# Kernel optimization log

Measured on AMD Instinct MI355X. Metric: run time of the kernel, lower is better.

Reference implementation:

```python
import jax, jax.numpy as jnp
import numpy as np

N = 100000      # nodes per node type
E = 500000      # edges per relation
DIN = 128
DOUT = 128
H = 8
DK = DOUT // H  # 16
SQRT_DK = float(np.sqrt(DK))


def setup_inputs() -> dict:
    key = jax.random.key(0)
    ks = jax.random.split(key, 24)
    s = 1.0 / np.sqrt(DIN)
    inp = {
        "h_a": jax.random.normal(ks[0], (N, DIN), jnp.float32),
        "h_b": jax.random.normal(ks[1], (N, DIN), jnp.float32),
        "src0": jax.random.randint(ks[2], (E,), 0, N, jnp.int32),
        "dst0": jax.random.randint(ks[3], (E,), 0, N, jnp.int32),
        "src1": jax.random.randint(ks[4], (E,), 0, N, jnp.int32),
        "dst1": jax.random.randint(ks[5], (E,), 0, N, jnp.int32),
        "src2": jax.random.randint(ks[6], (E,), 0, N, jnp.int32),
        "dst2": jax.random.randint(ks[7], (E,), 0, N, jnp.int32),
        "Wk": jax.random.normal(ks[8], (2, DIN, DOUT), jnp.float32) * s,
        "bk": jnp.zeros((2, DOUT), jnp.float32),
        "Wv": jax.random.normal(ks[9], (2, DIN, DOUT), jnp.float32) * s,
        "bv": jnp.zeros((2, DOUT), jnp.float32),
        "Wq": jax.random.normal(ks[10], (2, DIN, DOUT), jnp.float32) * s,
        "bq": jnp.zeros((2, DOUT), jnp.float32),
        "Wa": jax.random.normal(ks[11], (2, DOUT, DOUT), jnp.float32) * s,
        "ba": jnp.zeros((2, DOUT), jnp.float32),
        # xavier_uniform-like scale for [H, DK, DK] relation transforms
        "rel_att": jax.random.normal(ks[12], (3, H, DK, DK), jnp.float32) * (1.0 / np.sqrt(DK)),
        "rel_msg": jax.random.normal(ks[13], (3, H, DK, DK), jnp.float32) * (1.0 / np.sqrt(DK)),
        "rel_pri": 1.0 + 0.1 * jax.random.normal(ks[14], (3, H), jnp.float32),
        "skip": jnp.zeros((2,), jnp.float32),
    }
    return inp


def _relation(x_src, x_dst, src, dst, Wk_, bk_, Wv_, bv_, Wq_, bq_, att, msg, pri):
    """One canonical edge type: returns scatter-sum aggregation t [N, H, DK]."""
    k = (x_src @ Wk_ + bk_).reshape(-1, H, DK)
    k = jnp.einsum('nhd,hde->nhe', k, att)                     # relation-specific key transform
    v = jnp.einsum('nhd,hde->nhe', (x_src @ Wv_ + bv_).reshape(-1, H, DK), msg)
    q = (x_dst @ Wq_ + bq_).reshape(-1, H, DK)
    # per-edge dot-product score [E, H] (v_dot_u with q on dst, k on src)
    score = jnp.einsum('ehd,ehd->eh', q[dst], k[src]) * pri / SQRT_DK
    # edge softmax grouped by dst node
    smax = jax.ops.segment_max(score, dst, num_segments=N)
    smax = jnp.where(jnp.isfinite(smax), smax, 0.0)            # empty dst groups
    ex = jnp.exp(score - smax[dst])
    den = jax.ops.segment_sum(ex, dst, num_segments=N)
    a = ex / den[dst]                                          # [E, H]
    # message = v[src] * a, scatter-sum to dst
    return jax.ops.segment_sum(v[src] * a[..., None], dst, num_segments=N)


def reference(h_a, h_b, src0, dst0, src1, dst1, src2, dst2,
              Wk, bk, Wv, bv, Wq, bq, Wa, ba,
              rel_att, rel_msg, rel_pri, skip):
    # relations: 0: a->b, 1: b->a, 2: a->b
    t0 = _relation(h_a, h_b, src0, dst0, Wk[0], bk[0], Wv[0], bv[0], Wq[1], bq[1],
                   rel_att[0], rel_msg[0], rel_pri[0])
    t1 = _relation(h_b, h_a, src1, dst1, Wk[1], bk[1], Wv[1], bv[1], Wq[0], bq[0],
                   rel_att[1], rel_msg[1], rel_pri[1])
    t2 = _relation(h_a, h_b, src2, dst2, Wk[0], bk[0], Wv[0], bv[0], Wq[1], bq[1],
                   rel_att[2], rel_msg[2], rel_pri[2])
    t_a = t1.reshape(N, DOUT)                  # cross_reducer mean over 1 relation
    t_b = ((t0 + t2) * 0.5).reshape(N, DOUT)   # mean over 2 relations into type b

    def node_out(t, h, i):
        alpha = jax.nn.sigmoid(skip[i])
        o = t @ Wa[i] + ba[i]                  # dropout = identity (eval)
        return o * alpha + h * (1.0 - alpha)

    out_a = node_out(t_a, h_a, 0)
    out_b = node_out(t_b, h_b, 1)
    return jnp.stack([out_a, out_b])           # [2, N, DOUT]
```

## Files before the change

kernel.cpp:

```cpp
#include <hip/hip_runtime.h>
#include <math.h>

typedef short bf16x8 __attribute__((ext_vector_type(8)));
typedef float f32x4 __attribute__((ext_vector_type(4)));
typedef float f32x2 __attribute__((ext_vector_type(2)));

__device__ __forceinline__ unsigned short cvt_bf16(float f) {
    unsigned u = __float_as_uint(f);
    u += 0x7fffu + ((u >> 16) & 1);
    return (unsigned short)(u >> 16);
}
__device__ __forceinline__ float cvt_f32(unsigned short b) {
    return __uint_as_float(((unsigned)b) << 16);
}
__device__ __forceinline__ f32x2 bf16pair(unsigned u) {
    f32x2 r;
    r.x = __uint_as_float(u << 16);
    r.y = __uint_as_float(u & 0xffff0000u);
    return r;
}

__global__ void compose_kernel(const float* __restrict__ Wk, const float* __restrict__ bk,
                               const float* __restrict__ Wv, const float* __restrict__ bv,
                               const float* __restrict__ att, const float* __restrict__ msg,
                               const float* __restrict__ pri,
                               unsigned short* __restrict__ WkT, unsigned short* __restrict__ WvT,
                               float* __restrict__ bkC, float* __restrict__ bvC) {
    int tid = blockIdx.x * blockDim.x + threadIdx.x;
    if (tid >= 3 * 16384) return;
    int r = tid / 16384;
    int rem = tid & 16383;
    int c = rem >> 7;
    int i = rem & 127;
    int h = c >> 4, e = c & 15;
    int wsel = (r == 1) ? 1 : 0;
    float p = pri[r * 8 + h] * 0.25f;

    const float* wkrow = Wk + wsel * 16384 + i * 128 + h * 16;
    const float* wvrow = Wv + wsel * 16384 + i * 128 + h * 16;
    const float* attc = att + ((r * 8 + h) * 16) * 16 + e;
    const float* msgc = msg + ((r * 8 + h) * 16) * 16 + e;
    float aK = 0.f, aV = 0.f;
#pragma unroll
    for (int d = 0; d < 16; ++d) {
        aK += wkrow[d] * attc[d * 16];
        aV += wvrow[d] * msgc[d * 16];
    }
    WkT[r * 16384 + c * 128 + i] = cvt_bf16(aK * p);
    WvT[r * 16384 + c * 128 + i] = cvt_bf16(aV);
    if (i == 0) {
        const float* bkr = bk + wsel * 128 + h * 16;
        const float* bvr = bv + wsel * 128 + h * 16;
        float bK = 0.f, bV = 0.f;
#pragma unroll
        for (int d = 0; d < 16; ++d) {
            bK += bkr[d] * attc[d * 16];
            bV += bvr[d] * msgc[d * 16];
        }
        bkC[r * 128 + c] = bK * p;
        bvC[r * 128 + c] = bV;
    }
}

__global__ void tcast_kernel(const float* __restrict__ src, unsigned short* __restrict__ dst) {
    int tid = blockIdx.x * 256 + threadIdx.x;
    int c = tid >> 7, i = tid & 127;
    dst[tid] = cvt_bf16(src[i * 128 + c]);
}

__global__ void cast_kernel(const float* __restrict__ src, unsigned short* __restrict__ dst, int n4) {
    int t = blockIdx.x * 256 + threadIdx.x;
    if (t >= n4) return;
    float4 f = ((const float4*)src)[t];
    ushort4 o;
    o.x = cvt_bf16(f.x); o.y = cvt_bf16(f.y); o.z = cvt_bf16(f.z); o.w = cvt_bf16(f.w);
    ((ushort4*)dst)[t] = o;
}

struct OutSpec { const unsigned short* Wt; const float* bias; unsigned short* out; };
struct OutSpecs { OutSpec o[5]; };

#define LPAD 136

__global__ __launch_bounds__(256) void mfma_proj_kernel(const unsigned short* __restrict__ X,
                                                        int nrows, OutSpecs specs, int nout) {
    __shared__ unsigned short Xs[128 * LPAD];
    __shared__ unsigned short Ws[128 * LPAD];
    __shared__ float bs[128];
    int tid = threadIdx.x;
    int n0 = blockIdx.x * 128;
    int rows_in = nrows - n0; if (rows_in > 128) rows_in = 128;

    {
        int rowb = tid >> 4, seg = tid & 15;
#pragma unroll
        for (int p = 0; p < 8; ++p) {
            int row = p * 16 + rowb;
            int rowg = row < rows_in ? row : rows_in - 1;
            uint4 d = *(const uint4*)(X + ((size_t)(n0 + rowg)) * 128 + seg * 8);
            *(uint4*)&Xs[row * LPAD + seg * 8] = d;
        }
    }

    int wave = tid >> 6, lane = tid & 63;
    int l15 = lane & 15, quad = lane >> 4;

    for (int o = 0; o < nout; ++o) {
        {
            int rowb = tid >> 4, seg = tid & 15;
            const unsigned short* Wt = specs.o[o].Wt;
#pragma unroll
            for (int p = 0; p < 8; ++p) {
                int row = p * 16 + rowb;
                uint4 d = *(const uint4*)(Wt + (size_t)row * 128 + seg * 8);
                *(uint4*)&Ws[row * LPAD + seg * 8] = d;
            }
            if (tid < 128) bs[tid] = specs.o[o].bias[tid];
        }
        __syncthreads();

        f32x4 acc[2][8];
#pragma unroll
        for (int mi = 0; mi < 2; ++mi)
#pragma unroll
            for (int nt = 0; nt < 8; ++nt) acc[mi][nt] = (f32x4){0.f, 0.f, 0.f, 0.f};

#pragma unroll
        for (int ks = 0; ks < 4; ++ks) {
            bf16x8 afr[2];
            afr[0] = *(const bf16x8*)&Xs[(wave * 32 + l15) * LPAD + ks * 32 + quad * 8];
            afr[1] = *(const bf16x8*)&Xs[(wave * 32 + 16 + l15) * LPAD + ks * 32 + quad * 8];
#pragma unroll
            for (int nt = 0; nt < 8; ++nt) {
                bf16x8 bfr = *(const bf16x8*)&Ws[(nt * 16 + l15) * LPAD + ks * 32 + quad * 8];
                acc[0][nt] = __builtin_amdgcn_mfma_f32_16x16x32_bf16(afr[0], bfr, acc[0][nt], 0, 0, 0);
                acc[1][nt] = __builtin_amdgcn_mfma_f32_16x16x32_bf16(afr[1], bfr, acc[1][nt], 0, 0, 0);
            }
        }

        unsigned short* out = specs.o[o].out;
#pragma unroll
        for (int mi = 0; mi < 2; ++mi) {
            int rowbase = wave * 32 + mi * 16 + quad * 4;
#pragma unroll
            for (int r = 0; r < 4; ++r) {
                int row = rowbase + r;
                if (row < rows_in) {
#pragma unroll
                    for (int nt = 0; nt < 8; ++nt) {
                        int col = nt * 16 + l15;
                        out[(size_t)(n0 + row) * 128 + col] = cvt_bf16(acc[mi][nt][r] + bs[col]);
                    }
                }
            }
        }
        __syncthreads();
    }
}

__global__ __launch_bounds__(256) void mfma_out_kernel(const unsigned short* __restrict__ T16,
        int nrows, const unsigned short* __restrict__ WaT, const float* __restrict__ bias,
        const float* __restrict__ resid, const float* __restrict__ skipv, int skipidx,
        float* __restrict__ out) {
    __shared__ unsigned short Xs[128 * LPAD];
    __shared__ unsigned short Ws[128 * LPAD];
    __shared__ float bs[128];
    int tid = threadIdx.x;
    int n0 = blockIdx.x * 128;
    int rows_in = nrows - n0; if (rows_in > 128) rows_in = 128;

    {
        int rowb = tid >> 4, seg = tid & 15;
#pragma unroll
        for (int p = 0; p < 8; ++p) {
            int row = p * 16 + rowb;
            int rowg = row < rows_in ? row : rows_in - 1;
            uint4 d = *(const uint4*)(T16 + ((size_t)(n0 + rowg)) * 128 + seg * 8);
            *(uint4*)&Xs[row * LPAD + seg * 8] = d;
            uint4 w = *(const uint4*)(WaT + (size_t)row * 128 + seg * 8);
            *(uint4*)&Ws[row * LPAD + seg * 8] = w;
        }
        if (tid < 128) bs[tid] = bias[tid];
    }
    __syncthreads();

    int wave = tid >> 6, lane = tid & 63;
    int l15 = lane & 15, quad = lane >> 4;

    f32x4 acc[2][8];
#pragma unroll
    for (int mi = 0; mi < 2; ++mi)
#pragma unroll
        for (int nt = 0; nt < 8; ++nt) acc[mi][nt] = (f32x4){0.f, 0.f, 0.f, 0.f};

#pragma unroll
    for (int ks = 0; ks < 4; ++ks) {
        bf16x8 afr[2];
        afr[0] = *(const bf16x8*)&Xs[(wave * 32 + l15) * LPAD + ks * 32 + quad * 8];
        afr[1] = *(const bf16x8*)&Xs[(wave * 32 + 16 + l15) * LPAD + ks * 32 + quad * 8];
#pragma unroll
        for (int nt = 0; nt < 8; ++nt) {
            bf16x8 bfr = *(const bf16x8*)&Ws[(nt * 16 + l15) * LPAD + ks * 32 + quad * 8];
            acc[0][nt] = __builtin_amdgcn_mfma_f32_16x16x32_bf16(afr[0], bfr, acc[0][nt], 0, 0, 0);
            acc[1][nt] = __builtin_amdgcn_mfma_f32_16x16x32_bf16(afr[1], bfr, acc[1][nt], 0, 0, 0);
        }
    }

    float s = skipv[skipidx];
    float alpha = 1.f / (1.f + __expf(-s));
    float beta = 1.f - alpha;
#pragma unroll
    for (int mi = 0; mi < 2; ++mi) {
        int rowbase = wave * 32 + mi * 16 + quad * 4;
#pragma unroll
        for (int r = 0; r < 4; ++r) {
            int row = rowbase + r;
            if (row < rows_in) {
#pragma unroll
                for (int nt = 0; nt < 8; ++nt) {
                    int col = nt * 16 + l15;
                    size_t gi = (size_t)(n0 + row) * 128 + col;
                    out[gi] = alpha * (acc[mi][nt][r] + bs[col]) + beta * resid[gi];
                }
            }
        }
    }
}

__global__ void count_kernel(const int* __restrict__ dst, int* __restrict__ cnt, int E) {
    int e = blockIdx.x * 256 + threadIdx.x;
    if (e < E) atomicAdd(&cnt[dst[e]], 1);
}

#define SCAN_B 256
__global__ void scan1_kernel(const int* __restrict__ cnt, int* __restrict__ offs,
                             int* __restrict__ bsum, int n) {
    __shared__ int sh[SCAN_B];
    int i = blockIdx.x * SCAN_B + threadIdx.x;
    int v = (i < n) ? cnt[i] : 0;
    sh[threadIdx.x] = v;
    __syncthreads();
    for (int off = 1; off < SCAN_B; off <<= 1) {
        int t = (threadIdx.x >= off) ? sh[threadIdx.x - off] : 0;
        __syncthreads();
        sh[threadIdx.x] += t;
        __syncthreads();
    }
    if (i < n) offs[i] = sh[threadIdx.x] - v;
    if (threadIdx.x == SCAN_B - 1) bsum[blockIdx.x] = sh[threadIdx.x];
}

__global__ void scan2_kernel(int* __restrict__ bsum, int nb) {
    __shared__ int sh[512];
    int v = (threadIdx.x < nb) ? bsum[threadIdx.x] : 0;
    sh[threadIdx.x] = v;
    __syncthreads();
    for (int off = 1; off < 512; off <<= 1) {
        int t = (threadIdx.x >= off) ? sh[threadIdx.x - off] : 0;
        __syncthreads();
        sh[threadIdx.x] += t;
        __syncthreads();
    }
    if (threadIdx.x < nb) bsum[threadIdx.x] = sh[threadIdx.x] - v;
}

__global__ void scan3_kernel(int* __restrict__ offs, const int* __restrict__ bsum,
                             int* __restrict__ fill, int n) {
    int i = blockIdx.x * SCAN_B + threadIdx.x;
    if (i < n) {
        int o = offs[i] + bsum[blockIdx.x];
        offs[i] = o;
        fill[i] = o;
    }
}

__global__ void scatter_kernel(const int* __restrict__ src, const int* __restrict__ dst,
                               int* __restrict__ fill, int* __restrict__ ss, int E) {
    int e = blockIdx.x * 256 + threadIdx.x;
    if (e < E) {
        int p = atomicAdd(&fill[dst[e]], 1);
        ss[p] = src[e];
    }
}

struct AggSt { float den; f32x2 acc[8]; };

__device__ __forceinline__ void agg_loop(const unsigned short* __restrict__ k,
                                         const unsigned short* __restrict__ v,
                                         const int* __restrict__ ss,
                                         int start, int deg, int j, int h,
                                         const f32x2* q2, AggSt& st) {
    st.den = 0.f;
#pragma unroll
    for (int t = 0; t < 8; ++t) st.acc[t] = (f32x2){0.f, 0.f};
    for (int i = j; i < deg; i += 8) {
        int s = ss[start + i];
        const uint4* kp = (const uint4*)(k + (size_t)s * 128 + h * 16);
        uint4 ka = kp[0], kb = kp[1];
        const uint4* vp = (const uint4*)(v + (size_t)s * 128 + h * 16);
        uint4 va = vp[0], vb = vp[1];

        f32x2 d2 = (f32x2){0.f, 0.f};
        d2 += q2[0] * bf16pair(ka.x);
        d2 += q2[1] * bf16pair(ka.y);
        d2 += q2[2] * bf16pair(ka.z);
        d2 += q2[3] * bf16pair(ka.w);
        d2 += q2[4] * bf16pair(kb.x);
        d2 += q2[5] * bf16pair(kb.y);
        d2 += q2[6] * bf16pair(kb.z);
        d2 += q2[7] * bf16pair(kb.w);
        float sc = d2.x + d2.y;
        float ex = __expf(sc);
        st.den += ex;
        f32x2 exv = (f32x2){ex, ex};
        st.acc[0] += exv * bf16pair(va.x);
        st.acc[1] += exv * bf16pair(va.y);
        st.acc[2] += exv * bf16pair(va.z);
        st.acc[3] += exv * bf16pair(va.w);
        st.acc[4] += exv * bf16pair(vb.x);
        st.acc[5] += exv * bf16pair(vb.y);
        st.acc[6] += exv * bf16pair(vb.z);
        st.acc[7] += exv * bf16pair(vb.w);
    }
}

__device__ __forceinline__ void butterfly(AggSt& st) {
#pragma unroll
    for (int mask = 8; mask <= 32; mask <<= 1) {
        st.den += __shfl_xor(st.den, mask);
#pragma unroll
        for (int t = 0; t < 8; ++t) {
            st.acc[t].x += __shfl_xor(st.acc[t].x, mask);
            st.acc[t].y += __shfl_xor(st.acc[t].y, mask);
        }
    }
}

__device__ __forceinline__ void load_q(const unsigned short* __restrict__ q,
                                       int wid, int h, f32x2* q2) {
    const uint4* qp = (const uint4*)(q + (size_t)wid * 128 + h * 16);
    uint4 qa = qp[0], qb = qp[1];
    q2[0] = bf16pair(qa.x); q2[1] = bf16pair(qa.y);
    q2[2] = bf16pair(qa.z); q2[3] = bf16pair(qa.w);
    q2[4] = bf16pair(qb.x); q2[5] = bf16pair(qb.y);
    q2[6] = bf16pair(qb.z); q2[7] = bf16pair(qb.w);
}

__device__ __forceinline__ void store_bf16(unsigned short* __restrict__ outp,
                                           size_t base, const float* o) {
    unsigned short* op = outp + base;
    ushort4 p0, p1, p2, p3;
    p0.x = cvt_bf16(o[0]);  p0.y = cvt_bf16(o[1]);  p0.z = cvt_bf16(o[2]);  p0.w = cvt_bf16(o[3]);
    p1.x = cvt_bf16(o[4]);  p1.y = cvt_bf16(o[5]);  p1.z = cvt_bf16(o[6]);  p1.w = cvt_bf16(o[7]);
    p2.x = cvt_bf16(o[8]);  p2.y = cvt_bf16(o[9]);  p2.z = cvt_bf16(o[10]); p2.w = cvt_bf16(o[11]);
    p3.x = cvt_bf16(o[12]); p3.y = cvt_bf16(o[13]); p3.z = cvt_bf16(o[14]); p3.w = cvt_bf16(o[15]);
    ((ushort4*)op)[0] = p0; ((ushort4*)op)[1] = p1;
    ((ushort4*)op)[2] = p2; ((ushort4*)op)[3] = p3;
}

__global__ __launch_bounds__(256) void agg_fused_kernel(
    const unsigned short* __restrict__ qb,
    const unsigned short* __restrict__ k0, const unsigned short* __restrict__ v0,
    const int* __restrict__ offs0, const int* __restrict__ cnt0, const int* __restrict__ ss0,
    const unsigned short* __restrict__ k2, const unsigned short* __restrict__ v2,
    const int* __restrict__ offs2, const int* __restrict__ cnt2, const int* __restrict__ ss2,
    const unsigned short* __restrict__ qa,
    const unsigned short* __restrict__ k1, const unsigned short* __restrict__ v1,
    const int* __restrict__ offs1, const int* __restrict__ cnt1, const int* __restrict__ ss1,
    unsigned short* __restrict__ tb16, unsigned short* __restrict__ ta16,
    int N, int ablk) {
    int bid = blockIdx.x;
    int lane = threadIdx.x & 63;
    int j = lane >> 3, h = lane & 7;

    if (bid < ablk) {
        int wid = (bid * 256 + (int)threadIdx.x) >> 6;
        if (wid >= N) return;
        int start0 = offs0[wid], deg0 = cnt0[wid];
        int start2 = offs2[wid], deg2 = cnt2[wid];
        f32x2 q2[8];
        load_q(qb, wid, h, q2);

        AggSt s0, s2;
        agg_loop(k0, v0, ss0, start0, deg0, j, h, q2, s0);
        agg_loop(k2, v2, ss2, start2, deg2, j, h, q2, s2);
        butterfly(s0);
        butterfly(s2);

        if (j == 0) {
            float i0 = (deg0 > 0) ? (0.5f / s0.den) : 0.f;
            float i2 = (deg2 > 0) ? (0.5f / s2.den) : 0.f;
            float o[16];
#pragma unroll
            for (int t = 0; t < 8; ++t) {
                o[2 * t]     = s0.acc[t].x * i0 + s2.acc[t].x * i2;
                o[2 * t + 1] = s0.acc[t].y * i0 + s2.acc[t].y * i2;
            }
            store_bf16(tb16, (size_t)wid * 128 + h * 16, o);
        }
    } else {
        int wid = ((bid - ablk) * 256 + (int)threadIdx.x) >> 6;
        if (wid >= N) return;
        int start1 = offs1[wid], deg1 = cnt1[wid];
        f32x2 q2[8];
        load_q(qa, wid, h, q2);

        AggSt s1;
        agg_loop(k1, v1, ss1, start1, deg1, j, h, q2, s1);
        butterfly(s1);

        if (j == 0) {
            float i1 = (deg1 > 0) ? (1.0f / s1.den) : 0.f;
            float o[16];
#pragma unroll
            for (int t = 0; t < 8; ++t) {
                o[2 * t]     = s1.acc[t].x * i1;
                o[2 * t + 1] = s1.acc[t].y * i1;
            }
            store_bf16(ta16, (size_t)wid * 128 + h * 16, o);
        }
    }
}

extern "C" void kernel_launch(void* const* d_in, const int* in_sizes, int n_in,
                              void* d_out, int out_size, void* d_ws, size_t ws_size,
                              hipStream_t stream) {
    const float* h_a = (const float*)d_in[0];
    const float* h_b = (const float*)d_in[1];
    const int* srcs[3] = {(const int*)d_in[2], (const int*)d_in[4], (const int*)d_in[6]};
    const int* dsts[3] = {(const int*)d_in[3], (const int*)d_in[5], (const int*)d_in[7]};
    const float* Wk = (const float*)d_in[8];
    const float* bk = (const float*)d_in[9];
    const float* Wv = (const float*)d_in[10];
    const float* bv = (const float*)d_in[11];
    const float* Wq = (const float*)d_in[12];
    const float* bq = (const float*)d_in[13];
    const float* Wa = (const float*)d_in[14];
    const float* ba = (const float*)d_in[15];
    const float* att = (const float*)d_in[16];
    const float* msg = (const float*)d_in[17];
    const float* pri = (const float*)d_in[18];
    const float* skip = (const float*)d_in[19];

    const int N = in_sizes[0] / 128;
    const int E = in_sizes[2];
    const size_t NC = (size_t)N * 128;

    char* P = (char*)d_ws;
    auto alloc = [&](size_t bytes) { char* p = P; P += (bytes + 255) & ~(size_t)255; return p; };

    unsigned short* WkT = (unsigned short*)alloc(3 * 16384 * 2);
    unsigned short* WvT = (unsigned short*)alloc(3 * 16384 * 2);
    unsigned short* WqT = (unsigned short*)alloc(2 * 16384 * 2);
    unsigned short* WaT = (unsigned short*)alloc(2 * 16384 * 2);
    float* bkC = (float*)alloc(3 * 128 * 4);
    float* bvC = (float*)alloc(3 * 128 * 4);
    unsigned short* Xa16 = (unsigned short*)alloc(NC * 2);
    unsigned short* Xb16 = (unsigned short*)alloc(NC * 2);
    unsigned short* qa16 = (unsigned short*)alloc(NC * 2);
    unsigned short* qb16 = (unsigned short*)alloc(NC * 2);
    unsigned short* k16[3], *v16[3];
    for (int r = 0; r < 3; ++r) {
        k16[r] = (unsigned short*)alloc(NC * 2);
        v16[r] = (unsigned short*)alloc(NC * 2);
    }
    unsigned short* ta16 = (unsigned short*)alloc(NC * 2);
    unsigned short* tb16 = (unsigned short*)alloc(NC * 2);
    int *cnt[3], *offs[3], *fill[3], *ssb[3];
    for (int r = 0; r < 3; ++r) {
        cnt[r] = (int*)alloc((size_t)N * 4);
        offs[r] = (int*)alloc((size_t)N * 4);
        fill[r] = (int*)alloc((size_t)N * 4);
        ssb[r] = (int*)alloc((size_t)E * 4);
    }
    int* bsum = (int*)alloc(512 * 4);

    int eb = (E + 255) / 256;
    int scanb = (N + SCAN_B - 1) / SCAN_B;

    for (int r = 0; r < 3; ++r) {
        hipMemsetAsync(cnt[r], 0, (size_t)N * sizeof(int), stream);
        count_kernel<<<eb, 256, 0, stream>>>(dsts[r], cnt[r], E);
        scan1_kernel<<<scanb, SCAN_B, 0, stream>>>(cnt[r], offs[r], bsum, N);
        scan2_kernel<<<1, 512, 0, stream>>>(bsum, scanb);
        scan3_kernel<<<scanb, SCAN_B, 0, stream>>>(offs[r], bsum, fill[r], N);
        scatter_kernel<<<eb, 256, 0, stream>>>(srcs[r], dsts[r], fill[r], ssb[r], E);
    }

    compose_kernel<<<(3 * 16384 + 255) / 256, 256, 0, stream>>>(
        Wk, bk, Wv, bv, att, msg, pri, WkT, WvT, bkC, bvC);
    tcast_kernel<<<64, 256, 0, stream>>>(Wq, WqT);
    tcast_kernel<<<64, 256, 0, stream>>>(Wq + 16384, WqT + 16384);
    tcast_kernel<<<64, 256, 0, stream>>>(Wa, WaT);
    tcast_kernel<<<64, 256, 0, stream>>>(Wa + 16384, WaT + 16384);

    int n4 = (int)(NC / 4);
    cast_kernel<<<(n4 + 255) / 256, 256, 0, stream>>>(h_a, Xa16, n4);
    cast_kernel<<<(n4 + 255) / 256, 256, 0, stream>>>(h_b, Xb16, n4);

    int gblocks = (N + 127) / 128;

    OutSpecs sa;
    sa.o[0] = {WqT, bq, qa16};
    sa.o[1] = {WkT + 0 * 16384, bkC + 0 * 128, k16[0]};
    sa.o[2] = {WvT + 0 * 16384, bvC + 0 * 128, v16[0]};
    sa.o[3] = {WkT + 2 * 16384, bkC + 2 * 128, k16[2]};
    sa.o[4] = {WvT + 2 * 16384, bvC + 2 * 128, v16[2]};
    mfma_proj_kernel<<<gblocks, 256, 0, stream>>>(Xa16, N, sa, 5);

    OutSpecs sb;
    sb.o[0] = {WqT + 16384, bq + 128, qb16};
    sb.o[1] = {WkT + 1 * 16384, bkC + 1 * 128, k16[1]};
    sb.o[2] = {WvT + 1 * 16384, bvC + 1 * 128, v16[1]};
    sb.o[3] = {nullptr, nullptr, nullptr};
    sb.o[4] = {nullptr, nullptr, nullptr};
    mfma_proj_kernel<<<gblocks, 256, 0, stream>>>(Xb16, N, sb, 3);

    int ab = (N + 3) / 4;
    agg_fused_kernel<<<2 * ab, 256, 0, stream>>>(
        qb16, k16[0], v16[0], offs[0], cnt[0], ssb[0],
        k16[2], v16[2], offs[2], cnt[2], ssb[2],
        qa16, k16[1], v16[1], offs[1], cnt[1], ssb[1],
        tb16, ta16, N, ab);

    float* out = (float*)d_out;
    mfma_out_kernel<<<gblocks, 256, 0, stream>>>(ta16, N, WaT, ba, h_a, skip, 0, out);
    mfma_out_kernel<<<gblocks, 256, 0, stream>>>(tb16, N, WaT + 16384, ba + 128, h_b, skip, 1,
                                                 out + NC);
}
```

Baseline: 724.7 us.

## Batch per-relation and per-type kernels into single launches; half-wave aggregation per node

The three per-relation CSR build pipelines (memset, count, scan, scatter) are merged into single batched launches over concatenated buffers. The weight transposes, input casts, both projection kernels and both output kernels are each merged into one launch that selects its inputs by block index. The aggregation kernel now gives each destination node 32 lanes instead of 64 (4 edge slots by 8 heads), with a shorter butterfly reduction. This cuts launch count and serialization between small kernels and raises node-level parallelism in aggregation, at the cost of fewer lanes covering high-degree nodes.

```diff
diff --git a/kernel.cpp b/kernel.cpp
--- a/kernel.cpp
+++ b/kernel.cpp
@@ -62,33 +62,48 @@
     }
 }
 
-__global__ void tcast_kernel(const float* __restrict__ src, unsigned short* __restrict__ dst) {
+__global__ void tcast4_kernel(const float* __restrict__ Wq, const float* __restrict__ Wa,
+                              unsigned short* __restrict__ WqT, unsigned short* __restrict__ WaT) {
+    int m = blockIdx.y;
+    const float* src = (m < 2) ? Wq + m * 16384 : Wa + (m - 2) * 16384;
+    unsigned short* dst = (m < 2) ? WqT + m * 16384 : WaT + (m - 2) * 16384;
     int tid = blockIdx.x * 256 + threadIdx.x;
     int c = tid >> 7, i = tid & 127;
     dst[tid] = cvt_bf16(src[i * 128 + c]);
 }
 
-__global__ void cast_kernel(const float* __restrict__ src, unsigned short* __restrict__ dst, int n4) {
+__global__ void cast2_kernel(const float* __restrict__ a, const float* __restrict__ b,
+                             unsigned short* __restrict__ da, unsigned short* __restrict__ db,
+                             int n4) {
     int t = blockIdx.x * 256 + threadIdx.x;
-    if (t >= n4) return;
-    float4 f = ((const float4*)src)[t];
+    if (t >= 2 * n4) return;
+    int sel = t >= n4;
+    int i = sel ? t - n4 : t;
+    const float* s = sel ? b : a;
+    unsigned short* d = sel ? db : da;
+    float4 f = ((const float4*)s)[i];
     ushort4 o;
     o.x = cvt_bf16(f.x); o.y = cvt_bf16(f.y); o.z = cvt_bf16(f.z); o.w = cvt_bf16(f.w);
-    ((ushort4*)dst)[t] = o;
+    ((ushort4*)d)[i] = o;
 }
 
 struct OutSpec { const unsigned short* Wt; const float* bias; unsigned short* out; };
-struct OutSpecs { OutSpec o[5]; };
+struct OutSpecs8 { OutSpec o[8]; };
 
 #define LPAD 136
 
-__global__ __launch_bounds__(256) void mfma_proj_kernel(const unsigned short* __restrict__ X,
-                                                        int nrows, OutSpecs specs, int nout) {
+__global__ __launch_bounds__(256) void mfma_proj2_kernel(const unsigned short* __restrict__ Xa,
+                                                         const unsigned short* __restrict__ Xb,
+                                                         int nrows, OutSpecs8 specs, int gA) {
     __shared__ unsigned short Xs[128 * LPAD];
     __shared__ unsigned short Ws[128 * LPAD];
     __shared__ float bs[128];
     int tid = threadIdx.x;
-    int n0 = blockIdx.x * 128;
+    int aSide = blockIdx.x < gA;
+    const unsigned short* X = aSide ? Xa : Xb;
+    int obase = aSide ? 0 : 5;
+    int nout = aSide ? 5 : 3;
+    int n0 = (aSide ? blockIdx.x : blockIdx.x - gA) * 128;
     int rows_in = nrows - n0; if (rows_in > 128) rows_in = 128;
 
     {
@@ -105,17 +120,19 @@
     int wave = tid >> 6, lane = tid & 63;
     int l15 = lane & 15, quad = lane >> 4;
 
-    for (int o = 0; o < nout; ++o) {
+    for (int oo = 0; oo < nout; ++oo) {
+        const unsigned short* Wt = specs.o[obase + oo].Wt;
+        const float* bias = specs.o[obase + oo].bias;
+        unsigned short* out = specs.o[obase + oo].out;
         {
             int rowb = tid >> 4, seg = tid & 15;
-            const unsigned short* Wt = specs.o[o].Wt;
 #pragma unroll
             for (int p = 0; p < 8; ++p) {
                 int row = p * 16 + rowb;
                 uint4 d = *(const uint4*)(Wt + (size_t)row * 128 + seg * 8);
                 *(uint4*)&Ws[row * LPAD + seg * 8] = d;
             }
-            if (tid < 128) bs[tid] = specs.o[o].bias[tid];
+            if (tid < 128) bs[tid] = bias[tid];
         }
         __syncthreads();
 
@@ -138,7 +155,6 @@
             }
         }
 
-        unsigned short* out = specs.o[o].out;
 #pragma unroll
         for (int mi = 0; mi < 2; ++mi) {
             int rowbase = wave * 32 + mi * 16 + quad * 4;
@@ -158,15 +174,23 @@
     }
 }
 
-__global__ __launch_bounds__(256) void mfma_out_kernel(const unsigned short* __restrict__ T16,
-        int nrows, const unsigned short* __restrict__ WaT, const float* __restrict__ bias,
-        const float* __restrict__ resid, const float* __restrict__ skipv, int skipidx,
-        float* __restrict__ out) {
+__global__ __launch_bounds__(256) void mfma_out2_kernel(
+        const unsigned short* __restrict__ ta, const unsigned short* __restrict__ tb,
+        const unsigned short* __restrict__ WaT, const float* __restrict__ ba,
+        const float* __restrict__ h_a, const float* __restrict__ h_b,
+        const float* __restrict__ skipv, float* __restrict__ outbase,
+        int nrows, int gA) {
     __shared__ unsigned short Xs[128 * LPAD];
     __shared__ unsigned short Ws[128 * LPAD];
     __shared__ float bs[128];
     int tid = threadIdx.x;
-    int n0 = blockIdx.x * 128;
+    int sel = blockIdx.x >= gA;
+    int n0 = (sel ? blockIdx.x - gA : blockIdx.x) * 128;
+    const unsigned short* T16 = sel ? tb : ta;
+    const unsigned short* W = WaT + sel * 16384;
+    const float* bias = ba + sel * 128;
+    const float* resid = sel ? h_b : h_a;
+    float* out = outbase + (size_t)sel * nrows * 128;
     int rows_in = nrows - n0; if (rows_in > 128) rows_in = 128;
 
     {
@@ -177,7 +201,7 @@
             int rowg = row < rows_in ? row : rows_in - 1;
             uint4 d = *(const uint4*)(T16 + ((size_t)(n0 + rowg)) * 128 + seg * 8);
             *(uint4*)&Xs[row * LPAD + seg * 8] = d;
-            uint4 w = *(const uint4*)(WaT + (size_t)row * 128 + seg * 8);
+            uint4 w = *(const uint4*)(W + (size_t)row * 128 + seg * 8);
             *(uint4*)&Ws[row * LPAD + seg * 8] = w;
         }
         if (tid < 128) bs[tid] = bias[tid];
@@ -206,7 +230,7 @@
         }
     }
 
-    float s = skipv[skipidx];
+    float s = skipv[sel];
     float alpha = 1.f / (1.f + __expf(-s));
     float beta = 1.f - alpha;
 #pragma unroll
@@ -227,17 +251,24 @@
     }
 }
 
-__global__ void count_kernel(const int* __restrict__ dst, int* __restrict__ cnt, int E) {
-    int e = blockIdx.x * 256 + threadIdx.x;
-    if (e < E) atomicAdd(&cnt[dst[e]], 1);
+__global__ void count3_kernel(const int* __restrict__ d0, const int* __restrict__ d1,
+                              const int* __restrict__ d2, int* __restrict__ cnt3,
+                              int E, int N) {
+    int t = blockIdx.x * 256 + threadIdx.x;
+    if (t >= 3 * E) return;
+    int r = (t >= 2 * E) ? 2 : (t >= E ? 1 : 0);
+    int e = t - r * E;
+    const int* d = (r == 0) ? d0 : ((r == 1) ? d1 : d2);
+    atomicAdd(&cnt3[r * N + d[e]], 1);
 }
 
 #define SCAN_B 256
 __global__ void scan1_kernel(const int* __restrict__ cnt, int* __restrict__ offs,
                              int* __restrict__ bsum, int n) {
     __shared__ int sh[SCAN_B];
+    int rbase = blockIdx.y * n;
     int i = blockIdx.x * SCAN_B + threadIdx.x;
-    int v = (i < n) ? cnt[i] : 0;
+    int v = (i < n) ? cnt[rbase + i] : 0;
     sh[threadIdx.x] = v;
     __syncthreads();
     for (int off = 1; off < SCAN_B; off <<= 1) {
@@ -246,13 +277,14 @@
         sh[threadIdx.x] += t;
         __syncthreads();
     }
-    if (i < n) offs[i] = sh[threadIdx.x] - v;
-    if (threadIdx.x == SCAN_B - 1) bsum[blockIdx.x] = sh[threadIdx.x];
+    if (i < n) offs[rbase + i] = sh[threadIdx.x] - v;
+    if (threadIdx.x == SCAN_B - 1) bsum[blockIdx.y * 512 + blockIdx.x] = sh[threadIdx.x];
 }
 
 __global__ void scan2_kernel(int* __restrict__ bsum, int nb) {
     __shared__ int sh[512];
-    int v = (threadIdx.x < nb) ? bsum[threadIdx.x] : 0;
+    int* bs = bsum + blockIdx.x * 512;
+    int v = (threadIdx.x < nb) ? bs[threadIdx.x] : 0;
     sh[threadIdx.x] = v;
     __syncthreads();
     for (int off = 1; off < 512; off <<= 1) {
@@ -261,26 +293,33 @@
         sh[threadIdx.x] += t;
         __syncthreads();
     }
-    if (threadIdx.x < nb) bsum[threadIdx.x] = sh[threadIdx.x] - v;
+    if (threadIdx.x < nb) bs[threadIdx.x] = sh[threadIdx.x] - v;
 }
 
 __global__ void scan3_kernel(int* __restrict__ offs, const int* __restrict__ bsum,
                              int* __restrict__ fill, int n) {
+    int rbase = blockIdx.y * n;
     int i = blockIdx.x * SCAN_B + threadIdx.x;
     if (i < n) {
-        int o = offs[i] + bsum[blockIdx.x];
-        offs[i] = o;
-        fill[i] = o;
-    }
-}
-
-__global__ void scatter_kernel(const int* __restrict__ src, const int* __restrict__ dst,
-                               int* __restrict__ fill, int* __restrict__ ss, int E) {
-    int e = blockIdx.x * 256 + threadIdx.x;
-    if (e < E) {
-        int p = atomicAdd(&fill[dst[e]], 1);
-        ss[p] = src[e];
-    }
+        int o = offs[rbase + i] + bsum[blockIdx.y * 512 + blockIdx.x];
+        offs[rbase + i] = o;
+        fill[rbase + i] = o;
+    }
+}
+
+__global__ void scatter3_kernel(const int* __restrict__ s0, const int* __restrict__ d0,
+                                const int* __restrict__ s1, const int* __restrict__ d1,
+                                const int* __restrict__ s2, const int* __restrict__ d2,
+                                int* __restrict__ fill3, int* __restrict__ ss3,
+                                int E, int N) {
+    int t = blockIdx.x * 256 + threadIdx.x;
+    if (t >= 3 * E) return;
+    int r = (t >= 2 * E) ? 2 : (t >= E ? 1 : 0);
+    int e = t - r * E;
+    const int* sp = (r == 0) ? s0 : ((r == 1) ? s1 : s2);
+    const int* dp = (r == 0) ? d0 : ((r == 1) ? d1 : d2);
+    int p = atomicAdd(&fill3[r * N + dp[e]], 1);
+    ss3[(size_t)r * E + p] = sp[e];
 }
 
 struct AggSt { float den; f32x2 acc[8]; };
@@ -293,7 +332,7 @@
     st.den = 0.f;
 #pragma unroll
     for (int t = 0; t < 8; ++t) st.acc[t] = (f32x2){0.f, 0.f};
-    for (int i = j; i < deg; i += 8) {
+    for (int i = j; i < deg; i += 4) {
         int s = ss[start + i];
         const uint4* kp = (const uint4*)(k + (size_t)s * 128 + h * 16);
         uint4 ka = kp[0], kb = kp[1];
@@ -324,9 +363,9 @@
     }
 }
 
-__device__ __forceinline__ void butterfly(AggSt& st) {
-#pragma unroll
-    for (int mask = 8; mask <= 32; mask <<= 1) {
+__device__ __forceinline__ void butterfly32(AggSt& st) {
+#pragma unroll
+    for (int mask = 8; mask <= 16; mask <<= 1) {
         st.den += __shfl_xor(st.den, mask);
 #pragma unroll
         for (int t = 0; t < 8; ++t) {
@@ -368,13 +407,13 @@
     const unsigned short* __restrict__ k1, const unsigned short* __restrict__ v1,
     const int* __restrict__ offs1, const int* __restrict__ cnt1, const int* __restrict__ ss1,
     unsigned short* __restrict__ tb16, unsigned short* __restrict__ ta16,
-    int N, int ablk) {
+    int N, int bblk) {
     int bid = blockIdx.x;
-    int lane = threadIdx.x & 63;
-    int j = lane >> 3, h = lane & 7;
-
-    if (bid < ablk) {
-        int wid = (bid * 256 + (int)threadIdx.x) >> 6;
+    int l32 = threadIdx.x & 31;
+    int j = l32 >> 3, h = l32 & 7;
+
+    if (bid < bblk) {
+        int wid = (bid * 256 + (int)threadIdx.x) >> 5;
         if (wid >= N) return;
         int start0 = offs0[wid], deg0 = cnt0[wid];
         int start2 = offs2[wid], deg2 = cnt2[wid];
@@ -384,8 +423,8 @@
         AggSt s0, s2;
         agg_loop(k0, v0, ss0, start0, deg0, j, h, q2, s0);
         agg_loop(k2, v2, ss2, start2, deg2, j, h, q2, s2);
-        butterfly(s0);
-        butterfly(s2);
+        butterfly32(s0);
+        butterfly32(s2);
 
         if (j == 0) {
             float i0 = (deg0 > 0) ? (0.5f / s0.den) : 0.f;
@@ -399,7 +438,7 @@
             store_bf16(tb16, (size_t)wid * 128 + h * 16, o);
         }
     } else {
-        int wid = ((bid - ablk) * 256 + (int)threadIdx.x) >> 6;
+        int wid = ((bid - bblk) * 256 + (int)threadIdx.x) >> 5;
         if (wid >= N) return;
         int start1 = offs1[wid], deg1 = cnt1[wid];
         f32x2 q2[8];
@@ -407,7 +446,7 @@
 
         AggSt s1;
         agg_loop(k1, v1, ss1, start1, deg1, j, h, q2, s1);
-        butterfly(s1);
+        butterfly32(s1);
 
         if (j == 0) {
             float i1 = (deg1 > 0) ? (1.0f / s1.den) : 0.f;
@@ -466,65 +505,50 @@
     }
     unsigned short* ta16 = (unsigned short*)alloc(NC * 2);
     unsigned short* tb16 = (unsigned short*)alloc(NC * 2);
-    int *cnt[3], *offs[3], *fill[3], *ssb[3];
-    for (int r = 0; r < 3; ++r) {
-        cnt[r] = (int*)alloc((size_t)N * 4);
-        offs[r] = (int*)alloc((size_t)N * 4);
-        fill[r] = (int*)alloc((size_t)N * 4);
-        ssb[r] = (int*)alloc((size_t)E * 4);
-    }
-    int* bsum = (int*)alloc(512 * 4);
-
-    int eb = (E + 255) / 256;
+    int* cnt3 = (int*)alloc((size_t)3 * N * 4);
+    int* offs3 = (int*)alloc((size_t)3 * N * 4);
+    int* fill3 = (int*)alloc((size_t)3 * N * 4);
+    int* ss3 = (int*)alloc((size_t)3 * E * 4);
+    int* bsum = (int*)alloc(3 * 512 * 4);
+
+    int eb3 = (3 * E + 255) / 256;
     int scanb = (N + SCAN_B - 1) / SCAN_B;
 
-    for (int r = 0; r < 3; ++r) {
-        hipMemsetAsync(cnt[r], 0, (size_t)N * sizeof(int), stream);
-        count_kernel<<<eb, 256, 0, stream>>>(dsts[r], cnt[r], E);
-        scan1_kernel<<<scanb, SCAN_B, 0, stream>>>(cnt[r], offs[r], bsum, N);
-        scan2_kernel<<<1, 512, 0, stream>>>(bsum, scanb);
-        scan3_kernel<<<scanb, SCAN_B, 0, stream>>>(offs[r], bsum, fill[r], N);
-        scatter_kernel<<<eb, 256, 0, stream>>>(srcs[r], dsts[r], fill[r], ssb[r], E);
-    }
+    hipMemsetAsync(cnt3, 0, (size_t)3 * N * sizeof(int), stream);
+    count3_kernel<<<eb3, 256, 0, stream>>>(dsts[0], dsts[1], dsts[2], cnt3, E, N);
+    scan1_kernel<<<dim3(scanb, 3), SCAN_B, 0, stream>>>(cnt3, offs3, bsum, N);
+    scan2_kernel<<<3, 512, 0, stream>>>(bsum, scanb);
+    scan3_kernel<<<dim3(scanb, 3), SCAN_B, 0, stream>>>(offs3, bsum, fill3, N);
+    scatter3_kernel<<<eb3, 256, 0, stream>>>(srcs[0], dsts[0], srcs[1], dsts[1],
+                                             srcs[2], dsts[2], fill3, ss3, E, N);
 
     compose_kernel<<<(3 * 16384 + 255) / 256, 256, 0, stream>>>(
         Wk, bk, Wv, bv, att, msg, pri, WkT, WvT, bkC, bvC);
-    tcast_kernel<<<64, 256, 0, stream>>>(Wq, WqT);
-    tcast_kernel<<<64, 256, 0, stream>>>(Wq + 16384, WqT + 16384);
-    tcast_kernel<<<64, 256, 0, stream>>>(Wa, WaT);
-    tcast_kernel<<<64, 256, 0, stream>>>(Wa + 16384, WaT + 16384);
+    tcast4_kernel<<<dim3(64, 4), 256, 0, stream>>>(Wq, Wa, WqT, WaT);
 
     int n4 = (int)(NC / 4);
-    cast_kernel<<<(n4 + 255) / 256, 256, 0, stream>>>(h_a, Xa16, n4);
-    cast_kernel<<<(n4 + 255) / 256, 256, 0, stream>>>(h_b, Xb16, n4);
+    cast2_kernel<<<(2 * n4 + 255) / 256, 256, 0, stream>>>(h_a, h_b, Xa16, Xb16, n4);
 
     int gblocks = (N + 127) / 128;
 
-    OutSpecs sa;
-    sa.o[0] = {WqT, bq, qa16};
-    sa.o[1] = {WkT + 0 * 16384, bkC + 0 * 128, k16[0]};
-    sa.o[2] = {WvT + 0 * 16384, bvC + 0 * 128, v16[0]};
-    sa.o[3] = {WkT + 2 * 16384, bkC + 2 * 128, k16[2]};
-    sa.o[4] = {WvT + 2 * 16384, bvC + 2 * 128, v16[2]};
-    mfma_proj_kernel<<<gblocks, 256, 0, stream>>>(Xa16, N, sa, 5);
-
-    OutSpecs sb;
-    sb.o[0] = {WqT + 16384, bq + 128, qb16};
-    sb.o[1] = {WkT + 1 * 16384, bkC + 1 * 128, k16[1]};
-    sb.o[2] = {WvT + 1 * 16384, bvC + 1 * 128, v16[1]};
-    sb.o[3] = {nullptr, nullptr, nullptr};
-    sb.o[4] = {nullptr, nullptr, nullptr};
-    mfma_proj_kernel<<<gblocks, 256, 0, stream>>>(Xb16, N, sb, 3);
-
-    int ab = (N + 3) / 4;
-    agg_fused_kernel<<<2 * ab, 256, 0, stream>>>(
-        qb16, k16[0], v16[0], offs[0], cnt[0], ssb[0],
-        k16[2], v16[2], offs[2], cnt[2], ssb[2],
-        qa16, k16[1], v16[1], offs[1], cnt[1], ssb[1],
-        tb16, ta16, N, ab);
-
-    float* out = (float*)d_out;
-    mfma_out_kernel<<<gblocks, 256, 0, stream>>>(ta16, N, WaT, ba, h_a, skip, 0, out);
-    mfma_out_kernel<<<gblocks, 256, 0, stream>>>(tb16, N, WaT + 16384, ba + 128, h_b, skip, 1,
-                                                 out + NC);
-}
+    OutSpecs8 s8;
+    s8.o[0] = {WqT, bq, qa16};
+    s8.o[1] = {WkT + 0 * 16384, bkC + 0 * 128, k16[0]};
+    s8.o[2] = {WvT + 0 * 16384, bvC + 0 * 128, v16[0]};
+    s8.o[3] = {WkT + 2 * 16384, bkC + 2 * 128, k16[2]};
+    s8.o[4] = {WvT + 2 * 16384, bvC + 2 * 128, v16[2]};
+    s8.o[5] = {WqT + 16384, bq + 128, qb16};
+    s8.o[6] = {WkT + 1 * 16384, bkC + 1 * 128, k16[1]};
+    s8.o[7] = {WvT + 1 * 16384, bvC + 1 * 128, v16[1]};
+    mfma_proj2_kernel<<<2 * gblocks, 256, 0, stream>>>(Xa16, Xb16, N, s8, gblocks);
+
+    int bblk = (N + 7) / 8;
+    agg_fused_kernel<<<2 * bblk, 256, 0, stream>>>(
+        qb16, k16[0], v16[0], offs3 + 0 * N, cnt3 + 0 * N, ss3 + 0 * (size_t)E,
+        k16[2], v16[2], offs3 + 2 * N, cnt3 + 2 * N, ss3 + 2 * (size_t)E,
+        qa16, k16[1], v16[1], offs3 + 1 * N, cnt3 + 1 * N, ss3 + 1 * (size_t)E,
+        tb16, ta16, N, bblk);
+
+    mfma_out2_kernel<<<2 * gblocks, 256, 0, stream>>>(
+        ta16, tb16, WaT, ba, h_a, h_b, skip, (float*)d_out, N, gblocks);
+}
```

Result: faster. 654.4 us (-9.7%).
